# Kernel tuning notes

Measured on AMD Instinct MI355X. Metric: run time of the kernel, lower is better.

The kernel has to match this reference:

```python
import jax, jax.numpy as jnp
import numpy as np

LRELU = 0.1          # LeakyReLU negative slope
FLOAT_AMT = 0.1      # grid offset scale
BW_MIN, BW_MAX = 0.1, 0.5


def _grid_coors():
    gx = np.arange(-3.0, 3.0, 0.25)
    gy = np.arange(-3.0, 3.0, 0.25)
    gz = np.arange(-1.5, 1.5, 0.25)
    X, Y, Z = np.meshgrid(gx, gy, gz)
    xyz = np.stack([X.flatten(), Y.flatten(), Z.flatten()], axis=1)
    return jnp.asarray(xyz, dtype=jnp.float32)  # [N,3], N=6912


def _lin_init(k, fan_in, fan_out):
    kw, kb = jax.random.split(k)
    lim = 1.0 / np.sqrt(fan_in)
    W = jax.random.uniform(kw, (fan_in, fan_out), minval=-lim, maxval=lim, dtype=jnp.float32)
    b = jax.random.uniform(kb, (fan_out,), minval=-lim, maxval=lim, dtype=jnp.float32)
    return W, b


def setup_inputs() -> dict:
    key = jax.random.key(0)
    ks = jax.random.split(key, 16)
    B, S, IN_CH, GRID_CH, MID, NL = 16, 4096, 120, 64, 512, 6  # NL = num_block - 2
    grid_coors = _grid_coors()
    N = grid_coors.shape[0]

    proj_W, proj_b = _lin_init(ks[0], IN_CH + 2 * GRID_CH, MID)
    r1_W1, r1_b1 = _lin_init(ks[1], IN_CH + 128, MID)
    r1_W2, r1_b2 = _lin_init(ks[2], MID, MID)
    lw, lb = [], []
    for k in range(NL):
        W, b = _lin_init(ks[3 + k], MID, MID)
        lw.append(W); lb.append(b)
    layers_W = jnp.stack(lw)  # [6,512,512]
    layers_b = jnp.stack(lb)  # [6,512]
    out_W, out_b = _lin_init(ks[10], MID, 1)

    grid_0 = jax.random.normal(ks[11], (N, GRID_CH), dtype=jnp.float32) / np.sqrt(float(GRID_CH))
    xyz_offset = jnp.zeros((N, 3), dtype=jnp.float32)
    bandwidths = jnp.full((N,), 0.25, dtype=jnp.float32)

    input_stuff = jax.random.normal(ks[12], (B, S, IN_CH), dtype=jnp.float32)
    # positions inside the room bounds
    sound_loc = jax.random.uniform(ks[13], (B, 6), dtype=jnp.float32) * 3.0 - 1.5

    return dict(input_stuff=input_stuff, sound_loc=sound_loc, grid_coors=grid_coors,
                grid_0=grid_0, xyz_offset=xyz_offset, bandwidths=bandwidths,
                proj_W=proj_W, proj_b=proj_b, r1_W1=r1_W1, r1_b1=r1_b1,
                r1_W2=r1_W2, r1_b2=r1_b2, layers_W=layers_W, layers_b=layers_b,
                out_W=out_W, out_b=out_b)


def _leaky(x):
    return jnp.where(x >= 0, x, LRELU * x)


def _fit_predict(grid_pos, grid_feat, query, bw):
    d2 = jnp.sum((query[:, None, :] - grid_pos[None, :, :]) ** 2, axis=-1)  # [B,N]
    w = jax.nn.softmax(-d2 / (2.0 * bw[None, :] ** 2), axis=1)  # exp(-d^2/2bw^2) normalized
    return w @ grid_feat  # [B,C]


def reference(input_stuff, sound_loc, grid_coors, grid_0, xyz_offset, bandwidths,
              proj_W, proj_b, r1_W1, r1_b1, r1_W2, r1_b2, layers_W, layers_b,
              out_W, out_b):
    B, S, _ = input_stuff.shape
    bw = jnp.clip(bandwidths, BW_MIN, BW_MAX)
    grid_pos = grid_coors + jnp.tanh(xyz_offset) * FLOAT_AMT  # [N,3]

    f0 = _fit_predict(grid_pos, grid_0, sound_loc[:, :3], bw)  # [B,64]
    f1 = _fit_predict(grid_pos, grid_0, sound_loc[:, 3:], bw)  # [B,64]
    total_grid = jnp.broadcast_to(
        jnp.concatenate([f0, f1], axis=-1)[:, None, :], (B, S, 2 * f0.shape[-1]))
    my_input = jnp.concatenate([total_grid, input_stuff], axis=-1)  # [B,S,248]

    out = (my_input @ proj_W + proj_b)[:, :, None, :]  # [B,S,1,512]
    res = _leaky(my_input @ r1_W1 + r1_b1) @ r1_W2 + r1_b2  # [B,S,512]
    n = layers_W.shape[0]
    for k in range(n):
        out = _leaky(out) @ layers_W[k] + layers_b[k]
        if k == n // 2 - 1:
            out = out + res[:, :, None, :]
    return out @ out_W + out_b  # [B,S,1,1]
```

## Files before the change

### kernel.cpp

```cpp
#include <hip/hip_runtime.h>

#define LRELU 0.1f
#define MSTR 520

typedef _Float16 h4 __attribute__((ext_vector_type(4)));
typedef _Float16 h8 __attribute__((ext_vector_type(8)));
typedef float f4 __attribute__((ext_vector_type(4)));

struct KB8  { static constexpr int value = 8; };
struct KB16 { static constexpr int value = 16; };

__global__ __launch_bounds__(256) void k_gridfeat(
    const float* __restrict__ sound_loc, const float* __restrict__ grid_coors,
    const float* __restrict__ grid_0, const float* __restrict__ xyz_offset,
    const float* __restrict__ bandwidths, float* __restrict__ gf)
{
  const int N = 6912;
  __shared__ float s_lds[6912];
  __shared__ float red[256];
  int wg = blockIdx.x; int b = wg >> 1, q = wg & 1;
  int tid = threadIdx.x;
  float qx = sound_loc[b*6 + q*3 + 0];
  float qy = sound_loc[b*6 + q*3 + 1];
  float qz = sound_loc[b*6 + q*3 + 2];
  float lmax = -3.4e38f;
  for (int n = tid; n < N; n += 256) {
    float gx = grid_coors[n*3+0] + tanhf(xyz_offset[n*3+0]) * 0.1f;
    float gy = grid_coors[n*3+1] + tanhf(xyz_offset[n*3+1]) * 0.1f;
    float gz = grid_coors[n*3+2] + tanhf(xyz_offset[n*3+2]) * 0.1f;
    float bw = fminf(fmaxf(bandwidths[n], 0.1f), 0.5f);
    float dx = qx-gx, dy = qy-gy, dz = qz-gz;
    float d2 = dx*dx + dy*dy + dz*dz;
    float s = -d2 / (2.0f*bw*bw);
    s_lds[n] = s;
    lmax = fmaxf(lmax, s);
  }
  red[tid] = lmax; __syncthreads();
  for (int st = 128; st > 0; st >>= 1) {
    if (tid < st) red[tid] = fmaxf(red[tid], red[tid+st]);
    __syncthreads();
  }
  float mx = red[0]; __syncthreads();
  float lsum = 0.f;
  for (int n = tid; n < N; n += 256) {
    float e = expf(s_lds[n] - mx);
    s_lds[n] = e;
    lsum += e;
  }
  red[tid] = lsum; __syncthreads();
  for (int st = 128; st > 0; st >>= 1) {
    if (tid < st) red[tid] = red[tid] + red[tid+st];
    __syncthreads();
  }
  float total = red[0]; __syncthreads();
  int c = tid & 63, g = tid >> 6;
  float a0 = 0.f, a1 = 0.f, a2 = 0.f, a3 = 0.f;
  int n0 = g * 1728;
  for (int n = n0; n < n0 + 1728; n += 4) {
    a0 += s_lds[n+0] * grid_0[(n+0)*64 + c];
    a1 += s_lds[n+1] * grid_0[(n+1)*64 + c];
    a2 += s_lds[n+2] * grid_0[(n+2)*64 + c];
    a3 += s_lds[n+3] * grid_0[(n+3)*64 + c];
  }
  red[tid] = (a0 + a1) + (a2 + a3); __syncthreads();
  if (tid < 64) {
    float v = (red[tid] + red[tid+64] + red[tid+128] + red[tid+192]) / total;
    gf[b*128 + q*64 + tid] = v;
  }
}

__global__ __launch_bounds__(256) void k_pack(
    const float* __restrict__ r1W1, const float* __restrict__ projW,
    const float* __restrict__ r1W2, const float* __restrict__ layersW,
    _Float16* __restrict__ dst)
{
  __shared__ _Float16 T[512][40];
  int wg = blockIdx.x, t = threadIdx.x;
  const float* src; int K; long base; int kb;
  if (wg < 8)       { src = r1W1;  K = 248; base = 0;      kb = wg; }
  else if (wg < 16) { src = projW; K = 248; base = 131072; kb = wg - 8; }
  else if (wg < 32) { src = r1W2;  K = 512; base = 262144; kb = wg - 16; }
  else { int L = (wg - 32) >> 4; src = layersW + (long)L*262144;
         K = 512; base = 524288 + (long)L*262144; kb = (wg - 32) & 15; }
  for (int i4 = t; i4 < 4096; i4 += 256) {
    int kk = i4 >> 7, c4 = (i4 & 127) << 2;
    int k = kb*32 + kk;
    float4 v = (k < K) ? *(const float4*)&src[(long)k*512 + c4]
                       : make_float4(0.f, 0.f, 0.f, 0.f);
    T[c4+0][kk] = (_Float16)v.x; T[c4+1][kk] = (_Float16)v.y;
    T[c4+2][kk] = (_Float16)v.z; T[c4+3][kk] = (_Float16)v.w;
  }
  __syncthreads();
  _Float16* d = dst + base + (long)kb*32*512;
  for (int o = t; o < 2048; o += 256) {
    int nb = o >> 6, l = o & 63;
    h8 v = *(const h8*)&T[nb*16 + (l&15)][(l>>4) << 3];
    *(h8*)&d[(long)nb*512 + l*8] = v;
  }
}

__global__ __launch_bounds__(512, 2) void k_mlp(
    const float* __restrict__ input_stuff, const float* __restrict__ gf,
    const _Float16* __restrict__ wp,
    const float* __restrict__ proj_b, const float* __restrict__ r1_b1,
    const float* __restrict__ r1_b2, const float* __restrict__ layers_b,
    const float* __restrict__ out_W, const float* __restrict__ out_b,
    _Float16* __restrict__ res_spill, float* __restrict__ out)
{
  __shared__ _Float16 A[128 * MSTR];
  const int tid = threadIdx.x;
  const int w = tid >> 6, l = tid & 63;
  const long R0 = (long)blockIdx.x * 128;
  const int b = (int)(R0 >> 12);

  f4 acc[8][4];

  auto zero_acc = [&]() {
    #pragma unroll
    for (int mb = 0; mb < 8; ++mb)
      #pragma unroll
      for (int j = 0; j < 4; ++j)
        acc[mb][j] = (f4){0.f, 0.f, 0.f, 0.f};
  };

  auto stage_input = [&]() {
    const float* inp = input_stuff + R0 * 120;
    for (int i4 = tid; i4 < 3840; i4 += 512) {
      int m = i4 / 30, c4 = i4 - m * 30;
      float4 v = *(const float4*)&inp[(m*120 + c4*4)];
      h4 hv = { (_Float16)v.x, (_Float16)v.y, (_Float16)v.z, (_Float16)v.w };
      *(h4*)&A[m*MSTR + 128 + c4*4] = hv;
    }
    const float* g = gf + b * 128;
    for (int i4 = tid; i4 < 4096; i4 += 512) {
      int m = i4 >> 5, c4 = i4 & 31;
      float4 v = *(const float4*)&g[c4*4];
      h4 hv = { (_Float16)v.x, (_Float16)v.y, (_Float16)v.z, (_Float16)v.w };
      *(h4*)&A[m*MSTR + c4*4] = hv;
    }
    if (tid < 128) {
      h8 z = {};
      *(h8*)&A[tid*MSTR + 248] = z;
    }
  };

  auto matmul = [&](const _Float16* __restrict__ wbase, auto KBc) {
    constexpr int KB = KBc.value;
    const _Float16* abase = A + (l & 15)*MSTR + ((l >> 4) << 3);
    const h8* wb = (const h8*)wbase;
    h8 bb[2][4];
    #pragma unroll
    for (int j = 0; j < 4; ++j)
      bb[0][j] = wb[((w << 2) + j)*64 + l];
    #pragma unroll 2
    for (int kb = 0; kb < KB; ++kb) {
      if (kb + 1 < KB) {
        #pragma unroll
        for (int j = 0; j < 4; ++j)
          bb[(kb+1) & 1][j] = wb[((kb+1)*32 + (w << 2) + j)*64 + l];
      }
      h8 a[8];
      #pragma unroll
      for (int mb = 0; mb < 8; ++mb)
        a[mb] = *(const h8*)(abase + mb*16*MSTR + kb*32);
      #pragma unroll
      for (int j = 0; j < 4; ++j)
        #pragma unroll
        for (int mb = 0; mb < 8; ++mb)
          acc[mb][j] = __builtin_amdgcn_mfma_f32_16x16x32_f16(a[mb], bb[kb & 1][j], acc[mb][j], 0, 0, 0);
    }
  };

  _Float16* myres = res_spill + ((long)(blockIdx.x*8 + w)*64 + l) * 128;

  auto epilogue = [&](const float* bias, bool add_res, bool do_leaky) {
    h8 r0[8], r1[8];
    if (add_res) {
      #pragma unroll
      for (int mb = 0; mb < 8; ++mb) {
        r0[mb] = *(const h8*)(myres + mb*16);
        r1[mb] = *(const h8*)(myres + mb*16 + 8);
      }
    }
    #pragma unroll
    for (int mb = 0; mb < 8; ++mb) {
      int row0 = mb*16 + ((l >> 4) << 2);
      #pragma unroll
      for (int j = 0; j < 4; ++j) {
        int n = (w << 6) + (j << 4) + (l & 15);
        float bv = bias[n];
        #pragma unroll
        for (int r = 0; r < 4; ++r) {
          float v = acc[mb][j][r] + bv;
          if (add_res) {
            int idx = j*4 + r;
            v += (idx < 8) ? (float)r0[mb][idx] : (float)r1[mb][idx - 8];
          }
          if (do_leaky) v = (v >= 0.f) ? v : LRELU * v;
          A[(row0 + r)*MSTR + n] = (_Float16)v;
        }
      }
    }
  };

  auto epilogue_res = [&](const float* bias) {
    #pragma unroll
    for (int mb = 0; mb < 8; ++mb) {
      float vals[16];
      #pragma unroll
      for (int j = 0; j < 4; ++j) {
        int n = (w << 6) + (j << 4) + (l & 15);
        float bv = bias[n];
        #pragma unroll
        for (int r = 0; r < 4; ++r)
          vals[j*4 + r] = acc[mb][j][r] + bv;
      }
      h8 x0, x1;
      #pragma unroll
      for (int e = 0; e < 8; ++e) { x0[e] = (_Float16)vals[e]; x1[e] = (_Float16)vals[e+8]; }
      *(h8*)(myres + mb*16) = x0;
      *(h8*)(myres + mb*16 + 8) = x1;
    }
  };

  stage_input();
  __syncthreads();
  zero_acc(); matmul(wp + 0, KB8{});
  __syncthreads();
  epilogue(r1_b1, false, true);
  __syncthreads();
  zero_acc(); matmul(wp + 262144, KB16{});
  __syncthreads();
  epilogue_res(r1_b2);
  stage_input();
  __syncthreads();
  zero_acc(); matmul(wp + 131072, KB8{});
  __syncthreads();
  epilogue(proj_b, false, true);
  __syncthreads();
  for (int k = 0; k < 6; ++k) {
    zero_acc();
    matmul(wp + 524288 + (size_t)k*262144, KB16{});
    __syncthreads();
    epilogue(layers_b + k*512, k == 2, k < 5);
    __syncthreads();
  }
  {
    int r = tid >> 2, q = tid & 3;
    float s = 0.f;
    const _Float16* arow = &A[r*MSTR + q*128];
    const float* owq = out_W + q*128;
    for (int c = 0; c < 128; c += 4) {
      h4 v = *(const h4*)(arow + c);
      s += (float)v[0]*owq[c] + (float)v[1]*owq[c+1]
         + (float)v[2]*owq[c+2] + (float)v[3]*owq[c+3];
    }
    s += __shfl_xor(s, 1);
    s += __shfl_xor(s, 2);
    if (q == 0) out[R0 + r] = s + out_b[0];
  }
}

extern "C" void kernel_launch(void* const* d_in, const int* in_sizes, int n_in,
                              void* d_out, int out_size, void* d_ws, size_t ws_size,
                              hipStream_t stream) {
  const float* input_stuff = (const float*)d_in[0];
  const float* sound_loc   = (const float*)d_in[1];
  const float* grid_coors  = (const float*)d_in[2];
  const float* grid_0      = (const float*)d_in[3];
  const float* xyz_offset  = (const float*)d_in[4];
  const float* bandwidths  = (const float*)d_in[5];
  const float* proj_W  = (const float*)d_in[6];
  const float* proj_b  = (const float*)d_in[7];
  const float* r1_W1   = (const float*)d_in[8];
  const float* r1_b1   = (const float*)d_in[9];
  const float* r1_W2   = (const float*)d_in[10];
  const float* r1_b2   = (const float*)d_in[11];
  const float* layers_W = (const float*)d_in[12];
  const float* layers_b = (const float*)d_in[13];
  const float* out_W   = (const float*)d_in[14];
  const float* out_b   = (const float*)d_in[15];

  char* ws = (char*)d_ws;
  float*     gf  = (float*)ws;
  _Float16*  wp  = (_Float16*)(ws + (1 << 20));
  _Float16*  res = (_Float16*)(ws + (8 << 20));
  float* out = (float*)d_out;

  hipLaunchKernelGGL(k_gridfeat, dim3(32), dim3(256), 0, stream,
                     sound_loc, grid_coors, grid_0, xyz_offset, bandwidths, gf);
  hipLaunchKernelGGL(k_pack, dim3(128), dim3(256), 0, stream,
                     r1_W1, proj_W, r1_W2, layers_W, wp);
  hipLaunchKernelGGL(k_mlp, dim3(512), dim3(512), 0, stream,
                     input_stuff, gf, wp, proj_b, r1_b1, r1_b2, layers_b,
                     out_W, out_b, res, out);
}
```

Before: 461.9 us.

## Split grid regression into parallel kernels and vectorize MLP epilogue via transposed MFMA

The single 32-block grid-feature kernel becomes two kernels. The first computes normalized softmax weights into a workspace buffer, and the second spreads the weighted sum over grid_0 across 512 blocks, combining partial results with atomics into a zeroed buffer. In the MLP kernel, the MFMA operand order is swapped so each lane holds four consecutive output columns. That lets the epilogue use float4 bias loads, packed fp16 conversion and h4 stores into LDS. The costs are an extra memset and launch, plus non-deterministic atomic summation order.

```diff
diff --git a/kernel.cpp b/kernel.cpp
--- a/kernel.cpp
+++ b/kernel.cpp
@@ -5,20 +5,21 @@
 
 typedef _Float16 h4 __attribute__((ext_vector_type(4)));
 typedef _Float16 h8 __attribute__((ext_vector_type(8)));
+typedef __fp16 fp16x2 __attribute__((ext_vector_type(2)));
 typedef float f4 __attribute__((ext_vector_type(4)));
 
 struct KB8  { static constexpr int value = 8; };
 struct KB16 { static constexpr int value = 16; };
 
-__global__ __launch_bounds__(256) void k_gridfeat(
+__global__ __launch_bounds__(256) void k_gridA(
     const float* __restrict__ sound_loc, const float* __restrict__ grid_coors,
-    const float* __restrict__ grid_0, const float* __restrict__ xyz_offset,
-    const float* __restrict__ bandwidths, float* __restrict__ gf)
+    const float* __restrict__ xyz_offset, const float* __restrict__ bandwidths,
+    float* __restrict__ wn)
 {
   const int N = 6912;
   __shared__ float s_lds[6912];
   __shared__ float red[256];
-  int wg = blockIdx.x; int b = wg >> 1, q = wg & 1;
+  int bq = blockIdx.x; int b = bq >> 1, q = bq & 1;
   int tid = threadIdx.x;
   float qx = sound_loc[b*6 + q*3 + 0];
   float qy = sound_loc[b*6 + q*3 + 1];
@@ -30,8 +31,7 @@
     float gz = grid_coors[n*3+2] + tanhf(xyz_offset[n*3+2]) * 0.1f;
     float bw = fminf(fmaxf(bandwidths[n], 0.1f), 0.5f);
     float dx = qx-gx, dy = qy-gy, dz = qz-gz;
-    float d2 = dx*dx + dy*dy + dz*dz;
-    float s = -d2 / (2.0f*bw*bw);
+    float s = -(dx*dx + dy*dy + dz*dz) / (2.0f*bw*bw);
     s_lds[n] = s;
     lmax = fmaxf(lmax, s);
   }
@@ -52,20 +52,31 @@
     if (tid < st) red[tid] = red[tid] + red[tid+st];
     __syncthreads();
   }
-  float total = red[0]; __syncthreads();
-  int c = tid & 63, g = tid >> 6;
-  float a0 = 0.f, a1 = 0.f, a2 = 0.f, a3 = 0.f;
-  int n0 = g * 1728;
-  for (int n = n0; n < n0 + 1728; n += 4) {
-    a0 += s_lds[n+0] * grid_0[(n+0)*64 + c];
-    a1 += s_lds[n+1] * grid_0[(n+1)*64 + c];
-    a2 += s_lds[n+2] * grid_0[(n+2)*64 + c];
-    a3 += s_lds[n+3] * grid_0[(n+3)*64 + c];
-  }
-  red[tid] = (a0 + a1) + (a2 + a3); __syncthreads();
-  if (tid < 64) {
-    float v = (red[tid] + red[tid+64] + red[tid+128] + red[tid+192]) / total;
-    gf[b*128 + q*64 + tid] = v;
+  float inv = 1.0f / red[0]; __syncthreads();
+  for (int n = tid; n < N; n += 256)
+    wn[bq*6912 + n] = s_lds[n] * inv;
+}
+
+__global__ __launch_bounds__(256) void k_gridB(
+    const float* __restrict__ wn, const float* __restrict__ grid_0,
+    float* __restrict__ gf)
+{
+  int chunk = blockIdx.x, bq = blockIdx.y;
+  int t = threadIdx.x, c = t & 63, g = t >> 6;
+  int n0 = chunk*432 + g*108;
+  const float* wrow = wn + bq*6912 + n0;
+  const float* g0 = grid_0 + (long)n0*64 + c;
+  float a0 = 0.f, a1 = 0.f;
+  for (int i = 0; i < 108; i += 2) {
+    a0 += wrow[i]   * g0[(long)i*64];
+    a1 += wrow[i+1] * g0[(long)(i+1)*64];
+  }
+  __shared__ float red[256];
+  red[t] = a0 + a1; __syncthreads();
+  if (t < 64) {
+    float v = red[t] + red[t+64] + red[t+128] + red[t+192];
+    int b = bq >> 1, q = bq & 1;
+    atomicAdd(&gf[b*128 + q*64 + c], v);
   }
 }
 
@@ -110,6 +121,7 @@
   __shared__ _Float16 A[128 * MSTR];
   const int tid = threadIdx.x;
   const int w = tid >> 6, l = tid & 63;
+  const int q = l >> 4, r = l & 15;
   const long R0 = (long)blockIdx.x * 128;
   const int b = (int)(R0 >> 12);
 
@@ -146,7 +158,7 @@
 
   auto matmul = [&](const _Float16* __restrict__ wbase, auto KBc) {
     constexpr int KB = KBc.value;
-    const _Float16* abase = A + (l & 15)*MSTR + ((l >> 4) << 3);
+    const _Float16* abase = A + r*MSTR + (q << 3);
     const h8* wb = (const h8*)wbase;
     h8 bb[2][4];
     #pragma unroll
@@ -167,7 +179,8 @@
       for (int j = 0; j < 4; ++j)
         #pragma unroll
         for (int mb = 0; mb < 8; ++mb)
-          acc[mb][j] = __builtin_amdgcn_mfma_f32_16x16x32_f16(a[mb], bb[kb & 1][j], acc[mb][j], 0, 0, 0);
+          acc[mb][j] = __builtin_amdgcn_mfma_f32_16x16x32_f16(
+              bb[kb & 1][j], a[mb], acc[mb][j], 0, 0, 0);
     }
   };
 
@@ -183,22 +196,28 @@
       }
     }
     #pragma unroll
-    for (int mb = 0; mb < 8; ++mb) {
-      int row0 = mb*16 + ((l >> 4) << 2);
-      #pragma unroll
-      for (int j = 0; j < 4; ++j) {
-        int n = (w << 6) + (j << 4) + (l & 15);
-        float bv = bias[n];
-        #pragma unroll
-        for (int r = 0; r < 4; ++r) {
-          float v = acc[mb][j][r] + bv;
-          if (add_res) {
-            int idx = j*4 + r;
-            v += (idx < 8) ? (float)r0[mb][idx] : (float)r1[mb][idx - 8];
+    for (int j = 0; j < 4; ++j) {
+      float4 bv = *(const float4*)&bias[(w << 6) + (j << 4) + q*4];
+      #pragma unroll
+      for (int mb = 0; mb < 8; ++mb) {
+        f4 v = acc[mb][j];
+        v[0] += bv.x; v[1] += bv.y; v[2] += bv.z; v[3] += bv.w;
+        if (add_res) {
+          #pragma unroll
+          for (int s = 0; s < 4; ++s) {
+            int idx = j*4 + s;
+            v[s] += (idx < 8) ? (float)r0[mb][idx] : (float)r1[mb][idx - 8];
           }
-          if (do_leaky) v = (v >= 0.f) ? v : LRELU * v;
-          A[(row0 + r)*MSTR + n] = (_Float16)v;
         }
+        if (do_leaky) {
+          #pragma unroll
+          for (int s = 0; s < 4; ++s) v[s] = fmaxf(v[s], LRELU * v[s]);
+        }
+        fp16x2 p0 = __builtin_amdgcn_cvt_pkrtz(v[0], v[1]);
+        fp16x2 p1 = __builtin_amdgcn_cvt_pkrtz(v[2], v[3]);
+        h4 hv = { (_Float16)p0[0], (_Float16)p0[1],
+                  (_Float16)p1[0], (_Float16)p1[1] };
+        *(h4*)&A[(mb*16 + r)*MSTR + (w << 6) + (j << 4) + q*4] = hv;
       }
     }
   };
@@ -209,11 +228,11 @@
       float vals[16];
       #pragma unroll
       for (int j = 0; j < 4; ++j) {
-        int n = (w << 6) + (j << 4) + (l & 15);
-        float bv = bias[n];
-        #pragma unroll
-        for (int r = 0; r < 4; ++r)
-          vals[j*4 + r] = acc[mb][j][r] + bv;
+        float4 bv = *(const float4*)&bias[(w << 6) + (j << 4) + q*4];
+        vals[j*4+0] = acc[mb][j][0] + bv.x;
+        vals[j*4+1] = acc[mb][j][1] + bv.y;
+        vals[j*4+2] = acc[mb][j][2] + bv.z;
+        vals[j*4+3] = acc[mb][j][3] + bv.w;
       }
       h8 x0, x1;
       #pragma unroll
@@ -246,10 +265,10 @@
     __syncthreads();
   }
   {
-    int r = tid >> 2, q = tid & 3;
+    int rr = tid >> 2, qq = tid & 3;
     float s = 0.f;
-    const _Float16* arow = &A[r*MSTR + q*128];
-    const float* owq = out_W + q*128;
+    const _Float16* arow = &A[rr*MSTR + qq*128];
+    const float* owq = out_W + qq*128;
     for (int c = 0; c < 128; c += 4) {
       h4 v = *(const h4*)(arow + c);
       s += (float)v[0]*owq[c] + (float)v[1]*owq[c+1]
@@ -257,7 +276,7 @@
     }
     s += __shfl_xor(s, 1);
     s += __shfl_xor(s, 2);
-    if (q == 0) out[R0 + r] = s + out_b[0];
+    if (qq == 0) out[R0 + rr] = s + out_b[0];
   }
 }
 
@@ -283,12 +302,16 @@
 
   char* ws = (char*)d_ws;
   float*     gf  = (float*)ws;
+  float*     wn  = (float*)(ws + (64 << 10));
   _Float16*  wp  = (_Float16*)(ws + (1 << 20));
   _Float16*  res = (_Float16*)(ws + (8 << 20));
   float* out = (float*)d_out;
 
-  hipLaunchKernelGGL(k_gridfeat, dim3(32), dim3(256), 0, stream,
-                     sound_loc, grid_coors, grid_0, xyz_offset, bandwidths, gf);
+  (void)hipMemsetAsync(gf, 0, 16*128*sizeof(float), stream);
+  hipLaunchKernelGGL(k_gridA, dim3(32), dim3(256), 0, stream,
+                     sound_loc, grid_coors, xyz_offset, bandwidths, wn);
+  hipLaunchKernelGGL(k_gridB, dim3(16, 32), dim3(256), 0, stream,
+                     wn, grid_0, gf);
   hipLaunchKernelGGL(k_pack, dim3(128), dim3(256), 0, stream,
                      r1_W1, proj_W, r1_W2, layers_W, wp);
   hipLaunchKernelGGL(k_mlp, dim3(512), dim3(512), 0, stream,
```

New measurement: 418.8 us. -9.3%, faster.
